# Kernel tuning notes

Hardware: AMD Instinct MI355X
Metric: run time of the kernel (lower is better)

## Reference

```python
import jax, jax.numpy as jnp
import numpy as np

DIM = 4096
N_HEADS = 32
N_KV_HEADS = 8
HEAD_DIM = DIM // N_HEADS  # 128
SEQ = 2048
ROPE_THETA = 500000.0


def precompute_freqs_cis(head_dim, end, theta=ROPE_THETA):
    freq = 1.0 / theta ** (jnp.arange(0, head_dim, 2, dtype=jnp.float32) / head_dim)
    t = jnp.arange(end, dtype=jnp.float32)
    freqs = jnp.outer(t, freq)  # [S, D/2]
    return jnp.cos(freqs), jnp.sin(freqs)


def apply_rope(x, cos, sin):
    # x: [S, H, D]; cos/sin: [S, D/2]; interleaved even/odd rotation
    x_even = x[:, :, 0::2]
    x_odd = x[:, :, 1::2]
    c = cos[:, None, :]
    s = sin[:, None, :]
    rot_even = x_even * c - x_odd * s
    rot_odd = x_even * s + x_odd * c
    # re-interleave: stack on last axis then flatten -> [e0,o0,e1,o1,...]
    return jnp.stack([rot_even, rot_odd], axis=-1).reshape(x.shape)


def setup_inputs() -> dict:
    key = jax.random.key(0)
    ks = jax.random.split(key, 5)
    scale = 1.0 / np.sqrt(DIM)
    x = jax.random.normal(ks[0], (SEQ, DIM), dtype=jnp.float32)
    wq = jax.random.normal(ks[1], (DIM, DIM), dtype=jnp.float32) * scale
    wk = jax.random.normal(ks[2], (N_KV_HEADS * HEAD_DIM, DIM), dtype=jnp.float32) * scale
    wv = jax.random.normal(ks[3], (N_KV_HEADS * HEAD_DIM, DIM), dtype=jnp.float32) * scale
    wo = jax.random.normal(ks[4], (DIM, DIM), dtype=jnp.float32) * scale
    return {"x": x, "wq": wq, "wk": wk, "wv": wv, "wo": wo}


def reference(x, wq, wk, wv, wo):
    seq_len = x.shape[0]
    Q = (x @ wq.T).reshape(seq_len, N_HEADS, HEAD_DIM)
    K = (x @ wk.T).reshape(seq_len, N_KV_HEADS, HEAD_DIM)
    V = (x @ wv.T).reshape(seq_len, N_KV_HEADS, HEAD_DIM)
    cos, sin = precompute_freqs_cis(HEAD_DIM, seq_len)
    Q = apply_rope(Q, cos, sin)
    K = apply_rope(K, cos, sin)
    rep = N_HEADS // N_KV_HEADS
    K_rep = jnp.repeat(K, rep, axis=1)  # [S, H, D]
    V_rep = jnp.repeat(V, rep, axis=1)
    scores = jnp.einsum('qhd,khd->hqk', Q, K_rep) / np.sqrt(HEAD_DIM).astype(np.float32)
    causal = jnp.triu(jnp.ones((seq_len, seq_len), dtype=bool), k=1)
    scores = jnp.where(causal[None, :, :], -jnp.inf, scores)
    probs = jax.nn.softmax(scores.astype(jnp.float32), axis=-1).astype(Q.dtype)
    out = jnp.einsum('hqk,khd->qhd', probs, V_rep).reshape(seq_len, N_HEADS * HEAD_DIM)
    return out @ wo.T
```

## Files before the change

### kernel.cpp

```cpp
#include <hip/hip_runtime.h>
#include <stdint.h>
#include <math.h>

#define DIM 4096
#define NH 32
#define NKV 8
#define HD 128
#define SEQ 2048
#define KVDIM (NKV * HD)
#define QKVDIM (DIM + 2 * KVDIM)

typedef __bf16 bf16x8 __attribute__((ext_vector_type(8)));
typedef float floatx4 __attribute__((ext_vector_type(4)));
typedef uint16_t u16x8 __attribute__((ext_vector_type(8)));

#define AS1C(p) ((const __attribute__((address_space(1))) void*)(p))
#define AS3(p)  ((__attribute__((address_space(3))) void*)(p))

__device__ __forceinline__ float b2f(uint16_t u) {
    union { uint32_t i; float f; } v; v.i = ((uint32_t)u) << 16; return v.f;
}
__device__ __forceinline__ uint16_t f2b(float f) {
    union { float f; uint32_t i; } v; v.f = f;
    uint32_t r = v.i + 0x7fffu + ((v.i >> 16) & 1u);
    return (uint16_t)(r >> 16);
}

__device__ __forceinline__ u16x8 ldchunk(const void* p, bool isf32, size_t e) {
    if (isf32) {
        const float* fp = (const float*)p + e;
        u16x8 r;
#pragma unroll
        for (int j = 0; j < 8; ++j) r[j] = f2b(fp[j]);
        return r;
    }
    return *(const u16x8*)((const uint16_t*)p + e);
}

__global__ void detect_k(const uint16_t* __restrict__ x, int* __restrict__ flag) {
    __shared__ int cnt;
    if (threadIdx.x == 0) cnt = 0;
    __syncthreads();
    int bad = 0;
    for (int i = threadIdx.x; i < 4096; i += 256) {
        float v = b2f(x[i]);
        if (!(fabsf(v) < 1e6f)) bad++;
    }
    atomicAdd(&cnt, bad);
    __syncthreads();
    if (threadIdx.x == 0) *flag = (cnt > 256) ? 1 : 0;
}

__global__ __launch_bounds__(256) void conv_k(const void* __restrict__ src,
                                              uint16_t* __restrict__ dst,
                                              size_t n,
                                              const int* __restrict__ flagp) {
    const int f = *flagp;
    size_t i = ((size_t)blockIdx.x * blockDim.x + threadIdx.x) * 8;
    const size_t stride = (size_t)gridDim.x * blockDim.x * 8;
    if (f) {
        for (; i < n; i += stride) {
            const float* s = (const float*)src + i;
            u16x8 r;
#pragma unroll
            for (int j = 0; j < 8; ++j) r[j] = f2b(s[j]);
            *(u16x8*)(dst + i) = r;
        }
    } else {
        for (; i < n; i += stride)
            *(u16x8*)(dst + i) = *(const u16x8*)((const uint16_t*)src + i);
    }
}

__global__ __launch_bounds__(256) void conv4_k(const void* __restrict__ s0,
                                               const void* __restrict__ s1,
                                               const void* __restrict__ s2,
                                               const void* __restrict__ s3,
                                               uint16_t* __restrict__ d0,
                                               uint16_t* __restrict__ d1,
                                               uint16_t* __restrict__ d2,
                                               uint16_t* __restrict__ d3,
                                               size_t n0, size_t n1,
                                               size_t n2, size_t n3,
                                               const int* __restrict__ flagp) {
    const int f = *flagp;
    const size_t tot = (n0 + n1 + n2 + n3) >> 3;
    size_t c = (size_t)blockIdx.x * blockDim.x + threadIdx.x;
    const size_t stride = (size_t)gridDim.x * blockDim.x;
    for (; c < tot; c += stride) {
        size_t off = c << 3;
        const void* sp; uint16_t* dp;
        if (off < n0) { sp = s0; dp = d0; }
        else {
            off -= n0;
            if (off < n1) { sp = s1; dp = d1; }
            else {
                off -= n1;
                if (off < n2) { sp = s2; dp = d2; }
                else { off -= n2; sp = s3; dp = d3; }
            }
        }
        if (f) {
            const float* s = (const float*)sp + off;
            u16x8 r;
#pragma unroll
            for (int j = 0; j < 8; ++j) r[j] = f2b(s[j]);
            *(u16x8*)(dp + off) = r;
        } else {
            *(u16x8*)(dp + off) = *(const u16x8*)((const uint16_t*)sp + off);
        }
    }
}

__global__ __launch_bounds__(256) void gemm_nt(const void* __restrict__ A,
                                               const void* __restrict__ B,
                                               void* __restrict__ C,
                                               int K, int ldc,
                                               const int* __restrict__ flagp,
                                               int a_dyn, int b_dyn, int out_dyn,
                                               int out_trans) {
    __shared__ uint16_t As[128 * 64];
    __shared__ uint16_t Bs[128 * 64];
    const int f = *flagp;
    const bool af32 = a_dyn && f, bf32 = b_dyn && f, of32 = out_dyn && f;
    const int tid = threadIdx.x;
    const int wave = tid >> 6, lane = tid & 63;
    const int wh = wave >> 1, ww = wave & 1;
    const int quad = lane >> 4, l16 = lane & 15;
    const int m0 = blockIdx.x * 128;
    const int n0 = blockIdx.y * 128;

    floatx4 acc[4][4] = {};

    for (int k0 = 0; k0 < K; k0 += 64) {
        __syncthreads();
#pragma unroll
        for (int it = 0; it < 4; ++it) {
            int id = tid + it * 256;
            int row = id >> 3, slot = id & 7;
            int c8 = ((slot ^ (row & 7)) << 3);
            u16x8 va = ldchunk(A, af32, (size_t)(m0 + row) * K + k0 + c8);
            *(u16x8*)(As + row * 64 + slot * 8) = va;
            u16x8 vb = ldchunk(B, bf32, (size_t)(n0 + row) * K + k0 + c8);
            *(u16x8*)(Bs + row * 64 + slot * 8) = vb;
        }
        __syncthreads();
#pragma unroll
        for (int ks = 0; ks < 2; ++ks) {
            bf16x8 af[4], bf[4];
#pragma unroll
            for (int mi = 0; mi < 4; ++mi) {
                int r = wh * 64 + mi * 16 + l16;
                int slot = (ks * 4 + quad) ^ (r & 7);
                af[mi] = *(const bf16x8*)(As + r * 64 + slot * 8);
            }
#pragma unroll
            for (int ni = 0; ni < 4; ++ni) {
                int r = ww * 64 + ni * 16 + l16;
                int slot = (ks * 4 + quad) ^ (r & 7);
                bf[ni] = *(const bf16x8*)(Bs + r * 64 + slot * 8);
            }
#pragma unroll
            for (int mi = 0; mi < 4; ++mi)
#pragma unroll
                for (int ni = 0; ni < 4; ++ni)
                    acc[mi][ni] = __builtin_amdgcn_mfma_f32_16x16x32_bf16(
                        af[mi], bf[ni], acc[mi][ni], 0, 0, 0);
        }
    }
#pragma unroll
    for (int mi = 0; mi < 4; ++mi) {
#pragma unroll
        for (int ni = 0; ni < 4; ++ni) {
            int row = m0 + wh * 64 + mi * 16 + quad * 4;
            int col = n0 + ww * 64 + ni * 16 + l16;
            if (out_trans) {
                uint64_t pack = 0;
#pragma unroll
                for (int i = 0; i < 4; ++i)
                    pack |= (uint64_t)f2b(acc[mi][ni][i]) << (16 * i);
                *(uint64_t*)((uint16_t*)C + (size_t)col * ldc + row) = pack;
            } else if (of32) {
#pragma unroll
                for (int i = 0; i < 4; ++i)
                    ((float*)C)[(size_t)(row + i) * ldc + col] = acc[mi][ni][i];
            } else {
#pragma unroll
                for (int i = 0; i < 4; ++i)
                    ((uint16_t*)C)[(size_t)(row + i) * ldc + col] = f2b(acc[mi][ni][i]);
            }
        }
    }
}

__global__ __launch_bounds__(256) void gemm_bf(const uint16_t* __restrict__ A,
                                               const uint16_t* __restrict__ B,
                                               void* __restrict__ C,
                                               int K, int ldc,
                                               const int* __restrict__ flagp,
                                               int out_mode) {
    __shared__ uint16_t As[128 * 64];
    __shared__ uint16_t Bs[128 * 64];
    const bool of32 = (out_mode == 1) && (*flagp);
    const int tid = threadIdx.x;
    const int wave = tid >> 6, lane = tid & 63;
    const int wh = wave >> 1, ww = wave & 1;
    const int quad = lane >> 4, l16 = lane & 15;

    int nwg = gridDim.x * gridDim.y;
    int id = blockIdx.y * gridDim.x + blockIdx.x;
    if ((nwg & 7) == 0) {
        int cpx = nwg >> 3;
        id = (id & 7) * cpx + (id >> 3);
    }
    const int m0 = (id % gridDim.x) * 128;
    const int n0 = (id / gridDim.x) * 128;

    floatx4 acc[4][4] = {};

    for (int k0 = 0; k0 < K; k0 += 64) {
        __syncthreads();
#pragma unroll
        for (int it = 0; it < 4; ++it) {
            int idc = tid + it * 256;
            int row = idc >> 3, slot = idc & 7;
            int c8 = ((slot ^ (row & 7)) << 3);
            __builtin_amdgcn_global_load_lds(
                AS1C(A + (size_t)(m0 + row) * K + k0 + c8),
                AS3(As + (size_t)(it * 256 + wave * 64) * 8), 16, 0, 0);
            __builtin_amdgcn_global_load_lds(
                AS1C(B + (size_t)(n0 + row) * K + k0 + c8),
                AS3(Bs + (size_t)(it * 256 + wave * 64) * 8), 16, 0, 0);
        }
        __syncthreads();
#pragma unroll
        for (int ks = 0; ks < 2; ++ks) {
            bf16x8 af[4], bf[4];
#pragma unroll
            for (int mi = 0; mi < 4; ++mi) {
                int r = wh * 64 + mi * 16 + l16;
                int slot = (ks * 4 + quad) ^ (r & 7);
                af[mi] = *(const bf16x8*)(As + r * 64 + slot * 8);
            }
#pragma unroll
            for (int ni = 0; ni < 4; ++ni) {
                int r = ww * 64 + ni * 16 + l16;
                int slot = (ks * 4 + quad) ^ (r & 7);
                bf[ni] = *(const bf16x8*)(Bs + r * 64 + slot * 8);
            }
#pragma unroll
            for (int mi = 0; mi < 4; ++mi)
#pragma unroll
                for (int ni = 0; ni < 4; ++ni)
                    acc[mi][ni] = __builtin_amdgcn_mfma_f32_16x16x32_bf16(
                        af[mi], bf[ni], acc[mi][ni], 0, 0, 0);
        }
    }
#pragma unroll
    for (int mi = 0; mi < 4; ++mi) {
#pragma unroll
        for (int ni = 0; ni < 4; ++ni) {
            int row = m0 + wh * 64 + mi * 16 + quad * 4;
            int col = n0 + ww * 64 + ni * 16 + l16;
            if (of32) {
#pragma unroll
                for (int i = 0; i < 4; ++i)
                    ((float*)C)[(size_t)(row + i) * ldc + col] = acc[mi][ni][i];
            } else {
#pragma unroll
                for (int i = 0; i < 4; ++i)
                    ((uint16_t*)C)[(size_t)(row + i) * ldc + col] = f2b(acc[mi][ni][i]);
            }
        }
    }
}

__global__ __launch_bounds__(256) void gemm_qkv(const uint16_t* __restrict__ A,
                                                const uint16_t* __restrict__ W,
                                                uint16_t* __restrict__ Qo,
                                                uint16_t* __restrict__ Ko,
                                                uint16_t* __restrict__ VoT) {
    __shared__ uint16_t As[128 * 64];
    __shared__ uint16_t Bs[128 * 64];
    const int tid = threadIdx.x;
    const int wave = tid >> 6, lane = tid & 63;
    const int wh = wave >> 1, ww = wave & 1;
    const int quad = lane >> 4, l16 = lane & 15;

    int nwg = gridDim.x * gridDim.y;
    int id = blockIdx.y * gridDim.x + blockIdx.x;
    int cpx = nwg >> 3;
    id = (id & 7) * cpx + (id >> 3);
    const int m0 = (id % gridDim.x) * 128;
    const int n0 = (id / gridDim.x) * 128;
    const int K = DIM;

    floatx4 acc[4][4] = {};

    for (int k0 = 0; k0 < K; k0 += 64) {
        __syncthreads();
#pragma unroll
        for (int it = 0; it < 4; ++it) {
            int idc = tid + it * 256;
            int row = idc >> 3, slot = idc & 7;
            int c8 = ((slot ^ (row & 7)) << 3);
            __builtin_amdgcn_global_load_lds(
                AS1C(A + (size_t)(m0 + row) * K + k0 + c8),
                AS3(As + (size_t)(it * 256 + wave * 64) * 8), 16, 0, 0);
            __builtin_amdgcn_global_load_lds(
                AS1C(W + (size_t)(n0 + row) * K + k0 + c8),
                AS3(Bs + (size_t)(it * 256 + wave * 64) * 8), 16, 0, 0);
        }
        __syncthreads();
#pragma unroll
        for (int ks = 0; ks < 2; ++ks) {
            bf16x8 af[4], bf[4];
#pragma unroll
            for (int mi = 0; mi < 4; ++mi) {
                int r = wh * 64 + mi * 16 + l16;
                int slot = (ks * 4 + quad) ^ (r & 7);
                af[mi] = *(const bf16x8*)(As + r * 64 + slot * 8);
            }
#pragma unroll
            for (int ni = 0; ni < 4; ++ni) {
                int r = ww * 64 + ni * 16 + l16;
                int slot = (ks * 4 + quad) ^ (r & 7);
                bf[ni] = *(const bf16x8*)(Bs + r * 64 + slot * 8);
            }
#pragma unroll
            for (int mi = 0; mi < 4; ++mi)
#pragma unroll
                for (int ni = 0; ni < 4; ++ni)
                    acc[mi][ni] = __builtin_amdgcn_mfma_f32_16x16x32_bf16(
                        af[mi], bf[ni], acc[mi][ni], 0, 0, 0);
        }
    }
#pragma unroll
    for (int mi = 0; mi < 4; ++mi) {
#pragma unroll
        for (int ni = 0; ni < 4; ++ni) {
            int row = m0 + wh * 64 + mi * 16 + quad * 4;
            int col = n0 + ww * 64 + ni * 16 + l16;
            if (n0 < DIM) {
#pragma unroll
                for (int i = 0; i < 4; ++i)
                    Qo[(size_t)(row + i) * DIM + col] = f2b(acc[mi][ni][i]);
            } else if (n0 < DIM + KVDIM) {
                int c = col - DIM;
#pragma unroll
                for (int i = 0; i < 4; ++i)
                    Ko[(size_t)(row + i) * KVDIM + c] = f2b(acc[mi][ni][i]);
            } else {
                int c = col - DIM - KVDIM;
                uint64_t pack = 0;
#pragma unroll
                for (int i = 0; i < 4; ++i)
                    pack |= (uint64_t)f2b(acc[mi][ni][i]) << (16 * i);
                *(uint64_t*)(VoT + (size_t)c * SEQ + row) = pack;
            }
        }
    }
}

__global__ void rope2_k(uint16_t* __restrict__ Qb, uint16_t* __restrict__ Kb) {
    int id = blockIdx.x * blockDim.x + threadIdx.x;
    int i = id & 63;
    int rest = id >> 6;
    int hh = rest % (NH + NKV);
    int t = rest / (NH + NKV);
    uint16_t* p = (hh < NH)
        ? (Qb + (size_t)t * DIM + hh * HD + 2 * i)
        : (Kb + (size_t)t * KVDIM + (hh - NH) * HD + 2 * i);
    float e = b2f(p[0]), o = b2f(p[1]);
    float freq = exp2f(-(float)(2 * i) * (18.93156857f / 128.0f));
    float ang = (float)t * freq;
    float s, c;
    sincosf(ang, &s, &c);
    p[0] = f2b(e * c - o * s);
    p[1] = f2b(e * s + o * c);
}

__global__ __launch_bounds__(512, 4) void attn_k(const uint16_t* __restrict__ Q,
                                                 const uint16_t* __restrict__ Kg,
                                                 const uint16_t* __restrict__ VgT,
                                                 uint16_t* __restrict__ O) {
    __shared__ uint16_t Ks[2][64 * 128];
    __shared__ uint16_t Vt[2][128 * 64];
    __shared__ uint16_t Pb[128 * 64];

    const int tid = threadIdx.x;
    const int wave = tid >> 6, lane = tid & 63;
    const int quad = lane >> 4, l16 = lane & 15;

    const int head = blockIdx.x & 31;
    const int g16 = blockIdx.x >> 5;
    const int qt = (g16 < 8) ? (15 - g16) : (g16 - 8);
    const int kvh = head >> 2;
    const int q0 = qt * 128;
    const uint16_t* Vh = VgT + (size_t)kvh * HD * SEQ;

    const float scale = 0.08838834764831845f;
    const float LOG2E = 1.44269504f;

    auto stage_kv = [&](int buf, int k0s) {
#pragma unroll
        for (int it = 0; it < 2; ++it) {
            int id = tid + it * 512;
            int row = id >> 4, slot = id & 15;
            int c8 = ((slot ^ (row & 7)) << 3);
            __builtin_amdgcn_global_load_lds(
                AS1C(Kg + (size_t)(k0s + row) * KVDIM + kvh * HD + c8),
                AS3(Ks[buf] + (size_t)(it * 512 + wave * 64) * 8), 16, 0, 0);
        }
#pragma unroll
        for (int it = 0; it < 2; ++it) {
            int id = tid + it * 512;
            int d = id >> 3, slot = id & 7;
            int c8 = ((slot ^ (d & 7)) << 3);
            __builtin_amdgcn_global_load_lds(
                AS1C(Vh + (size_t)d * SEQ + k0s + c8),
                AS3(Vt[buf] + (size_t)(it * 512 + wave * 64) * 8), 16, 0, 0);
        }
    };

    bf16x8 qf[4];
    {
        const uint16_t* qrow = Q + (size_t)(q0 + wave * 16 + l16) * DIM + head * HD;
#pragma unroll
        for (int ks = 0; ks < 4; ++ks)
            qf[ks] = *(const bf16x8*)(qrow + (ks * 4 + quad) * 8);
    }

    floatx4 acc_o[8] = {};
    float m_run[4], l_run[4];
#pragma unroll
    for (int i = 0; i < 4; ++i) { m_run[i] = -__builtin_inff(); l_run[i] = 0.f; }

    const int nkt = 2 * qt + 2;
    stage_kv(0, 0);
    __syncthreads();

    for (int t = 0; t < nkt; ++t) {
        const int k0 = t * 64;
        const bool diag = (t >= 2 * qt);
        const int cur = t & 1;

        if (t + 1 < nkt) stage_kv((t + 1) & 1, (t + 1) * 64);
        __builtin_amdgcn_sched_barrier(0);

        floatx4 acc_s[4] = {};
        __builtin_amdgcn_s_setprio(1);
#pragma unroll
        for (int ks = 0; ks < 4; ++ks) {
            bf16x8 kf[4];
#pragma unroll
            for (int ni = 0; ni < 4; ++ni) {
                int r = ni * 16 + l16;
                int slot = (ks * 4 + quad) ^ (r & 7);
                kf[ni] = *(const bf16x8*)(Ks[cur] + r * 128 + slot * 8);
            }
#pragma unroll
            for (int ni = 0; ni < 4; ++ni)
                acc_s[ni] = __builtin_amdgcn_mfma_f32_16x16x32_bf16(
                    qf[ks], kf[ni], acc_s[ni], 0, 0, 0);
        }
        __builtin_amdgcn_s_setprio(0);

#pragma unroll
        for (int ni = 0; ni < 4; ++ni)
#pragma unroll
            for (int i = 0; i < 4; ++i) {
                float s = acc_s[ni][i] * scale;
                if (diag) {
                    int ql = q0 + wave * 16 + quad * 4 + i;
                    int kl = k0 + ni * 16 + l16;
                    if (kl > ql) s = -__builtin_inff();
                }
                acc_s[ni][i] = s;
            }

        float alpha[4];
#pragma unroll
        for (int i = 0; i < 4; ++i) {
            float v = fmaxf(fmaxf(acc_s[0][i], acc_s[1][i]),
                            fmaxf(acc_s[2][i], acc_s[3][i]));
#pragma unroll
            for (int off = 1; off < 16; off <<= 1)
                v = fmaxf(v, __shfl_xor(v, off));
            float mn = fmaxf(m_run[i], v);
            alpha[i] = exp2f((m_run[i] - mn) * LOG2E);
            m_run[i] = mn;

            int ql = wave * 16 + quad * 4 + i;
            float sum = 0.f;
#pragma unroll
            for (int ni = 0; ni < 4; ++ni) {
                float p = exp2f((acc_s[ni][i] - mn) * LOG2E);
                sum += p;
                int key = ni * 16 + l16;
                int slot = ((key >> 3) ^ (ql & 7) ^ ((ql >> 3) & 7)) & 7;
                Pb[ql * 64 + slot * 8 + (key & 7)] = f2b(p);
            }
#pragma unroll
            for (int off = 1; off < 16; off <<= 1)
                sum += __shfl_xor(sum, off);
            l_run[i] = l_run[i] * alpha[i] + sum;
        }

#pragma unroll
        for (int ni = 0; ni < 8; ++ni)
#pragma unroll
            for (int i = 0; i < 4; ++i)
                acc_o[ni][i] *= alpha[i];

        __builtin_amdgcn_s_setprio(1);
#pragma unroll
        for (int ks2 = 0; ks2 < 2; ++ks2) {
            bf16x8 pf, vf[8];
            {
                int r = wave * 16 + l16;
                int slot = ((ks2 * 4 + quad) ^ (r & 7) ^ ((r >> 3) & 7)) & 7;
                pf = *(const bf16x8*)(Pb + r * 64 + slot * 8);
            }
#pragma unroll
            for (int ni = 0; ni < 8; ++ni) {
                int d = ni * 16 + l16;
                int slot = ((ks2 * 4 + quad) ^ (d & 7)) & 7;
                vf[ni] = *(const bf16x8*)(Vt[cur] + d * 64 + slot * 8);
            }
#pragma unroll
            for (int ni = 0; ni < 8; ++ni)
                acc_o[ni] = __builtin_amdgcn_mfma_f32_16x16x32_bf16(
                    pf, vf[ni], acc_o[ni], 0, 0, 0);
        }
        __builtin_amdgcn_s_setprio(0);

        __syncthreads();
    }

#pragma unroll
    for (int i = 0; i < 4; ++i) {
        float inv = 1.0f / l_run[i];
        int row = q0 + wave * 16 + quad * 4 + i;
#pragma unroll
        for (int ni = 0; ni < 8; ++ni) {
            int col = head * HD + ni * 16 + l16;
            O[(size_t)row * DIM + col] = f2b(acc_o[ni][i] * inv);
        }
    }
}

extern "C" void kernel_launch(void* const* d_in, const int* in_sizes, int n_in,
                              void* d_out, int out_size, void* d_ws, size_t ws_size,
                              hipStream_t stream) {
    const void* x  = d_in[0];
    const void* wq = d_in[1];
    const void* wk = d_in[2];
    const void* wv = d_in[3];
    const void* wo = d_in[4];

    int* flag = (int*)d_ws;
    uint16_t* Kb  = (uint16_t*)((char*)d_ws + 256);
    uint16_t* VbT = Kb + (size_t)SEQ * KVDIM;
    uint16_t* xb  = VbT + (size_t)SEQ * KVDIM;
    uint16_t* BIG = xb + (size_t)SEQ * DIM;
    uint16_t* Wqkv = BIG;
    uint16_t* Ab   = BIG;
    uint16_t* Wo   = BIG + (size_t)SEQ * DIM;
    uint16_t* Qb = (uint16_t*)d_out;

    const size_t need = 256 + ((size_t)2 * SEQ * KVDIM
                             + (size_t)SEQ * DIM
                             + (size_t)QKVDIM * DIM) * 2;

    dim3 blk(256);
    detect_k<<<1, blk, 0, stream>>>((const uint16_t*)x, flag);

    if (ws_size >= need) {
        conv4_k<<<4096, blk, 0, stream>>>(
            x, wq, wk, wv,
            xb, Wqkv, Wqkv + (size_t)DIM * DIM, Wqkv + (size_t)(DIM + KVDIM) * DIM,
            (size_t)SEQ * DIM, (size_t)DIM * DIM,
            (size_t)KVDIM * DIM, (size_t)KVDIM * DIM, flag);
        gemm_qkv<<<dim3(SEQ / 128, QKVDIM / 128), blk, 0, stream>>>(
            xb, Wqkv, Qb, Kb, VbT);
        conv_k<<<2048, blk, 0, stream>>>(wo, Wo, (size_t)DIM * DIM, flag);
        rope2_k<<<(SEQ * (NH + NKV) * 64) / 256, 256, 0, stream>>>(Qb, Kb);
        attn_k<<<NH * 16, dim3(512), 0, stream>>>(Qb, Kb, VbT, Ab);
        gemm_bf<<<dim3(SEQ / 128, DIM / 128), blk, 0, stream>>>(Ab, Wo, d_out, DIM, DIM, flag, 1);
    } else {
        uint16_t* AbL = xb;
        gemm_nt<<<dim3(SEQ / 128, DIM / 128), blk, 0, stream>>>(x, wq, Qb, DIM, DIM, flag, 1, 1, 0, 0);
        gemm_nt<<<dim3(SEQ / 128, KVDIM / 128), blk, 0, stream>>>(x, wk, Kb, DIM, KVDIM, flag, 1, 1, 0, 0);
        gemm_nt<<<dim3(SEQ / 128, KVDIM / 128), blk, 0, stream>>>(x, wv, VbT, DIM, SEQ, flag, 1, 1, 0, 1);
        rope2_k<<<(SEQ * (NH + NKV) * 64) / 256, 256, 0, stream>>>(Qb, Kb);
        attn_k<<<NH * 16, dim3(512), 0, stream>>>(Qb, Kb, VbT, AbL);
        gemm_nt<<<dim3(SEQ / 128, DIM / 128), blk, 0, stream>>>(AbL, wo, d_out, DIM, DIM, flag, 0, 1, 1, 0);
    }
}
```

Baseline: 520.8 us.

## Pair causal query tiles per block and transpose score MFMA with lazy rescale

Each attention block now processes two query tiles (qt and 15-qt) sequentially, so every block does equal causal work and the grid shrinks from 512 to 256 blocks. The KV staging pipeline carries across the two halves. The S=K·Q^T MFMA operand order is swapped so each lane owns one query row, which removes most cross-lane shuffles in the softmax reductions. The output rescale is skipped unless some row's max grows by more than a threshold. Risks: half the blocks on a 256-CU part, serialized tiles per block, and launch bounds relaxed to one block per CU, which may raise register use and reduce occupancy.

```diff
diff --git a/kernel.cpp b/kernel.cpp
--- a/kernel.cpp
+++ b/kernel.cpp
@@ -380,7 +380,7 @@
     p[1] = f2b(e * s + o * c);
 }
 
-__global__ __launch_bounds__(512, 4) void attn_k(const uint16_t* __restrict__ Q,
+__global__ __launch_bounds__(512, 1) void attn_k(const uint16_t* __restrict__ Q,
                                                  const uint16_t* __restrict__ Kg,
                                                  const uint16_t* __restrict__ VgT,
                                                  uint16_t* __restrict__ O) {
@@ -393,10 +393,8 @@
     const int quad = lane >> 4, l16 = lane & 15;
 
     const int head = blockIdx.x & 31;
-    const int g16 = blockIdx.x >> 5;
-    const int qt = (g16 < 8) ? (15 - g16) : (g16 - 8);
+    const int pairid = blockIdx.x >> 5;
     const int kvh = head >> 2;
-    const int q0 = qt * 128;
     const uint16_t* Vh = VgT + (size_t)kvh * HD * SEQ;
 
     const float scale = 0.08838834764831845f;
@@ -423,129 +421,155 @@
         }
     };
 
-    bf16x8 qf[4];
-    {
-        const uint16_t* qrow = Q + (size_t)(q0 + wave * 16 + l16) * DIM + head * HD;
-#pragma unroll
-        for (int ks = 0; ks < 4; ++ks)
-            qf[ks] = *(const bf16x8*)(qrow + (ks * 4 + quad) * 8);
-    }
-
-    floatx4 acc_o[8] = {};
-    float m_run[4], l_run[4];
-#pragma unroll
-    for (int i = 0; i < 4; ++i) { m_run[i] = -__builtin_inff(); l_run[i] = 0.f; }
-
-    const int nkt = 2 * qt + 2;
+    int g = 0;
     stage_kv(0, 0);
     __syncthreads();
 
-    for (int t = 0; t < nkt; ++t) {
-        const int k0 = t * 64;
-        const bool diag = (t >= 2 * qt);
-        const int cur = t & 1;
-
-        if (t + 1 < nkt) stage_kv((t + 1) & 1, (t + 1) * 64);
-        __builtin_amdgcn_sched_barrier(0);
-
-        floatx4 acc_s[4] = {};
-        __builtin_amdgcn_s_setprio(1);
-#pragma unroll
-        for (int ks = 0; ks < 4; ++ks) {
-            bf16x8 kf[4];
-#pragma unroll
-            for (int ni = 0; ni < 4; ++ni) {
-                int r = ni * 16 + l16;
-                int slot = (ks * 4 + quad) ^ (r & 7);
-                kf[ni] = *(const bf16x8*)(Ks[cur] + r * 128 + slot * 8);
-            }
+    for (int half = 0; half < 2; ++half) {
+        const int qt = half ? (15 - pairid) : pairid;
+        const int q0 = qt * 128;
+        const int nkt = 2 * qt + 2;
+        const int qrow_l = q0 + wave * 16 + l16;
+
+        bf16x8 qf[4];
+        {
+            const uint16_t* qrow = Q + (size_t)qrow_l * DIM + head * HD;
+#pragma unroll
+            for (int ks = 0; ks < 4; ++ks)
+                qf[ks] = *(const bf16x8*)(qrow + (ks * 4 + quad) * 8);
+        }
+
+        floatx4 acc_o[8] = {};
+        float m_run = -__builtin_inff(), l_run = 0.f;
+
+        for (int t = 0; t < nkt; ++t, ++g) {
+            const int k0 = t * 64;
+            const bool diag = (t >= 2 * qt);
+            const int cur = g & 1;
+
+            if (!(half == 1 && t == nkt - 1)) {
+                int k0n = (t + 1 < nkt) ? (t + 1) * 64 : 0;
+                stage_kv((g + 1) & 1, k0n);
+            }
+            __builtin_amdgcn_sched_barrier(0);
+
+            floatx4 acc_s[4] = {};
+            __builtin_amdgcn_s_setprio(1);
+#pragma unroll
+            for (int ks = 0; ks < 4; ++ks) {
+                bf16x8 kf[4];
+#pragma unroll
+                for (int ni = 0; ni < 4; ++ni) {
+                    int r = ni * 16 + l16;
+                    int slot = (ks * 4 + quad) ^ (r & 7);
+                    kf[ni] = *(const bf16x8*)(Ks[cur] + r * 128 + slot * 8);
+                }
+#pragma unroll
+                for (int ni = 0; ni < 4; ++ni)
+                    acc_s[ni] = __builtin_amdgcn_mfma_f32_16x16x32_bf16(
+                        kf[ni], qf[ks], acc_s[ni], 0, 0, 0);
+            }
+            __builtin_amdgcn_s_setprio(0);
+
 #pragma unroll
             for (int ni = 0; ni < 4; ++ni)
-                acc_s[ni] = __builtin_amdgcn_mfma_f32_16x16x32_bf16(
-                    qf[ks], kf[ni], acc_s[ni], 0, 0, 0);
-        }
-        __builtin_amdgcn_s_setprio(0);
-
-#pragma unroll
-        for (int ni = 0; ni < 4; ++ni)
+#pragma unroll
+                for (int i = 0; i < 4; ++i) {
+                    float s = acc_s[ni][i] * scale;
+                    if (diag) {
+                        int kl = k0 + ni * 16 + quad * 4 + i;
+                        if (kl > qrow_l) s = -__builtin_inff();
+                    }
+                    acc_s[ni][i] = s;
+                }
+
+            float pmax;
+            {
+                float v0 = fmaxf(fmaxf(acc_s[0][0], acc_s[0][1]), fmaxf(acc_s[0][2], acc_s[0][3]));
+                float v1 = fmaxf(fmaxf(acc_s[1][0], acc_s[1][1]), fmaxf(acc_s[1][2], acc_s[1][3]));
+                float v2 = fmaxf(fmaxf(acc_s[2][0], acc_s[2][1]), fmaxf(acc_s[2][2], acc_s[2][3]));
+                float v3 = fmaxf(fmaxf(acc_s[3][0], acc_s[3][1]), fmaxf(acc_s[3][2], acc_s[3][3]));
+                pmax = fmaxf(fmaxf(v0, v1), fmaxf(v2, v3));
+                pmax = fmaxf(pmax, __shfl_xor(pmax, 16));
+                pmax = fmaxf(pmax, __shfl_xor(pmax, 32));
+            }
+
+            if (__any(pmax > m_run + 8.0f)) {
+                float mn = fmaxf(m_run, pmax);
+                float alpha = exp2f((m_run - mn) * LOG2E);
+                m_run = mn;
+                l_run *= alpha;
+                float aq[4];
+#pragma unroll
+                for (int i = 0; i < 4; ++i)
+                    aq[i] = __shfl(alpha, quad * 4 + i);
+#pragma unroll
+                for (int ni = 0; ni < 8; ++ni)
+#pragma unroll
+                    for (int i = 0; i < 4; ++i)
+                        acc_o[ni][i] *= aq[i];
+            }
+
+            {
+                const int ql = wave * 16 + l16;
+                const int swz = (ql & 7) ^ ((ql >> 3) & 7);
+                uint16_t* prow = Pb + ql * 64;
+                float sum = 0.f;
+#pragma unroll
+                for (int ni = 0; ni < 4; ++ni)
+#pragma unroll
+                    for (int i = 0; i < 4; ++i) {
+                        float p = exp2f((acc_s[ni][i] - m_run) * LOG2E);
+                        sum += p;
+                        int key = ni * 16 + quad * 4 + i;
+                        int slot = ((key >> 3) ^ swz) & 7;
+                        prow[slot * 8 + (key & 7)] = f2b(p);
+                    }
+                sum += __shfl_xor(sum, 16);
+                sum += __shfl_xor(sum, 32);
+                l_run += sum;
+            }
+
+            __builtin_amdgcn_s_setprio(1);
+#pragma unroll
+            for (int ks2 = 0; ks2 < 2; ++ks2) {
+                bf16x8 pf, vf[8];
+                {
+                    int r = wave * 16 + l16;
+                    int slot = ((ks2 * 4 + quad) ^ (r & 7) ^ ((r >> 3) & 7)) & 7;
+                    pf = *(const bf16x8*)(Pb + r * 64 + slot * 8);
+                }
+#pragma unroll
+                for (int ni = 0; ni < 8; ++ni) {
+                    int d = ni * 16 + l16;
+                    int slot = ((ks2 * 4 + quad) ^ (d & 7)) & 7;
+                    vf[ni] = *(const bf16x8*)(Vt[cur] + d * 64 + slot * 8);
+                }
+#pragma unroll
+                for (int ni = 0; ni < 8; ++ni)
+                    acc_o[ni] = __builtin_amdgcn_mfma_f32_16x16x32_bf16(
+                        pf, vf[ni], acc_o[ni], 0, 0, 0);
+            }
+            __builtin_amdgcn_s_setprio(0);
+
+            __syncthreads();
+        }
+
+        {
+            float inv = 1.0f / l_run;
+            float invq[4];
+#pragma unroll
+            for (int i = 0; i < 4; ++i)
+                invq[i] = __shfl(inv, quad * 4 + i);
 #pragma unroll
             for (int i = 0; i < 4; ++i) {
-                float s = acc_s[ni][i] * scale;
-                if (diag) {
-                    int ql = q0 + wave * 16 + quad * 4 + i;
-                    int kl = k0 + ni * 16 + l16;
-                    if (kl > ql) s = -__builtin_inff();
+                int row = q0 + wave * 16 + quad * 4 + i;
+#pragma unroll
+                for (int ni = 0; ni < 8; ++ni) {
+                    int col = head * HD + ni * 16 + l16;
+                    O[(size_t)row * DIM + col] = f2b(acc_o[ni][i] * invq[i]);
                 }
-                acc_s[ni][i] = s;
-            }
-
-        float alpha[4];
-#pragma unroll
-        for (int i = 0; i < 4; ++i) {
-            float v = fmaxf(fmaxf(acc_s[0][i], acc_s[1][i]),
-                            fmaxf(acc_s[2][i], acc_s[3][i]));
-#pragma unroll
-            for (int off = 1; off < 16; off <<= 1)
-                v = fmaxf(v, __shfl_xor(v, off));
-            float mn = fmaxf(m_run[i], v);
-            alpha[i] = exp2f((m_run[i] - mn) * LOG2E);
-            m_run[i] = mn;
-
-            int ql = wave * 16 + quad * 4 + i;
-            float sum = 0.f;
-#pragma unroll
-            for (int ni = 0; ni < 4; ++ni) {
-                float p = exp2f((acc_s[ni][i] - mn) * LOG2E);
-                sum += p;
-                int key = ni * 16 + l16;
-                int slot = ((key >> 3) ^ (ql & 7) ^ ((ql >> 3) & 7)) & 7;
-                Pb[ql * 64 + slot * 8 + (key & 7)] = f2b(p);
-            }
-#pragma unroll
-            for (int off = 1; off < 16; off <<= 1)
-                sum += __shfl_xor(sum, off);
-            l_run[i] = l_run[i] * alpha[i] + sum;
-        }
-
-#pragma unroll
-        for (int ni = 0; ni < 8; ++ni)
-#pragma unroll
-            for (int i = 0; i < 4; ++i)
-                acc_o[ni][i] *= alpha[i];
-
-        __builtin_amdgcn_s_setprio(1);
-#pragma unroll
-        for (int ks2 = 0; ks2 < 2; ++ks2) {
-            bf16x8 pf, vf[8];
-            {
-                int r = wave * 16 + l16;
-                int slot = ((ks2 * 4 + quad) ^ (r & 7) ^ ((r >> 3) & 7)) & 7;
-                pf = *(const bf16x8*)(Pb + r * 64 + slot * 8);
-            }
-#pragma unroll
-            for (int ni = 0; ni < 8; ++ni) {
-                int d = ni * 16 + l16;
-                int slot = ((ks2 * 4 + quad) ^ (d & 7)) & 7;
-                vf[ni] = *(const bf16x8*)(Vt[cur] + d * 64 + slot * 8);
-            }
-#pragma unroll
-            for (int ni = 0; ni < 8; ++ni)
-                acc_o[ni] = __builtin_amdgcn_mfma_f32_16x16x32_bf16(
-                    pf, vf[ni], acc_o[ni], 0, 0, 0);
-        }
-        __builtin_amdgcn_s_setprio(0);
-
-        __syncthreads();
-    }
-
-#pragma unroll
-    for (int i = 0; i < 4; ++i) {
-        float inv = 1.0f / l_run[i];
-        int row = q0 + wave * 16 + quad * 4 + i;
-#pragma unroll
-        for (int ni = 0; ni < 8; ++ni) {
-            int col = head * HD + ni * 16 + l16;
-            O[(size_t)row * DIM + col] = f2b(acc_o[ni][i] * inv);
+            }
         }
     }
 }
@@ -586,7 +610,7 @@
             xb, Wqkv, Qb, Kb, VbT);
         conv_k<<<2048, blk, 0, stream>>>(wo, Wo, (size_t)DIM * DIM, flag);
         rope2_k<<<(SEQ * (NH + NKV) * 64) / 256, 256, 0, stream>>>(Qb, Kb);
-        attn_k<<<NH * 16, dim3(512), 0, stream>>>(Qb, Kb, VbT, Ab);
+        attn_k<<<NH * 8, dim3(512), 0, stream>>>(Qb, Kb, VbT, Ab);
         gemm_bf<<<dim3(SEQ / 128, DIM / 128), blk, 0, stream>>>(Ab, Wo, d_out, DIM, DIM, flag, 1);
     } else {
         uint16_t* AbL = xb;
@@ -594,7 +618,7 @@
         gemm_nt<<<dim3(SEQ / 128, KVDIM / 128), blk, 0, stream>>>(x, wk, Kb, DIM, KVDIM, flag, 1, 1, 0, 0);
         gemm_nt<<<dim3(SEQ / 128, KVDIM / 128), blk, 0, stream>>>(x, wv, VbT, DIM, SEQ, flag, 1, 1, 0, 1);
         rope2_k<<<(SEQ * (NH + NKV) * 64) / 256, 256, 0, stream>>>(Qb, Kb);
-        attn_k<<<NH * 16, dim3(512), 0, stream>>>(Qb, Kb, VbT, AbL);
+        attn_k<<<NH * 8, dim3(512), 0, stream>>>(Qb, Kb, VbT, AbL);
         gemm_nt<<<dim3(SEQ / 128, DIM / 128), blk, 0, stream>>>(AbL, wo, d_out, DIM, DIM, flag, 0, 1, 1, 0);
     }
 }
```

Result: faster. 494.4 us (-5.1%).
